# Kernel optimization log

Hardware: AMD Instinct MI355X
Metric: run time of the kernel (lower is better)

The kernel has to match this reference:

```python
import jax, jax.numpy as jnp
import numpy as np

NUM_GRAPHS = 512   # number of graphs in the batch
MAX_NODES = 192    # static pad bound (actual sizes are in [96,160])
TOTAL = 65536      # total atoms across all graphs
D = 256            # model dim (from MultiheadAttention(256, 4))
H = 4              # heads
DH = D // H        # head dim = 64


def setup_inputs() -> dict:
    # Ragged graph sizes that sum exactly to TOTAL (pairs 128+p / 128-p).
    rng = np.random.default_rng(0)
    p = rng.integers(0, 33, size=NUM_GRAPHS // 2)
    sizes = np.concatenate([128 + p, 128 - p])
    rng.shuffle(sizes)
    batch = np.repeat(np.arange(NUM_GRAPHS, dtype=np.int32), sizes)

    key = jax.random.key(0)
    ks = jax.random.split(key, 12)
    s = 0.02
    return {
        "x": jax.random.normal(ks[0], (TOTAL, D), jnp.float32),
        "batch": jnp.asarray(batch),
        # attn1 (torch MultiheadAttention packed in_proj + out_proj)
        "in_w1": jax.random.normal(ks[1], (3 * D, D), jnp.float32) * s,
        "in_b1": jnp.zeros((3 * D,), jnp.float32),
        "out_w1": jax.random.normal(ks[2], (D, D), jnp.float32) * s,
        "out_b1": jnp.zeros((D,), jnp.float32),
        # attn2
        "in_w2": jax.random.normal(ks[3], (3 * D, D), jnp.float32) * s,
        "in_b2": jnp.zeros((3 * D,), jnp.float32),
        "out_w2": jax.random.normal(ks[4], (D, D), jnp.float32) * s,
        "out_b2": jnp.zeros((D,), jnp.float32),
        # readout MLP: 256 -> 256 -> 128 -> 1 (dropout is identity in eval)
        "r_w1": jax.random.normal(ks[5], (256, 256), jnp.float32) * s,
        "r_b1": jnp.zeros((256,), jnp.float32),
        "r_w2": jax.random.normal(ks[6], (128, 256), jnp.float32) * s,
        "r_b2": jnp.zeros((128,), jnp.float32),
        "r_w3": jax.random.normal(ks[7], (1, 128), jnp.float32) * s,
        "r_b3": jnp.zeros((1,), jnp.float32),
    }


def _mha(xd, mask, in_w, in_b, out_w, out_b):
    # xd: [B, L, D], mask: [B, L] (True = valid key). torch MHA semantics.
    B, L, _ = xd.shape
    qkv = xd @ in_w.T + in_b                                  # [B, L, 3D]
    q, k, v = jnp.split(qkv, 3, axis=-1)
    split = lambda t: t.reshape(B, L, H, DH).transpose(0, 2, 1, 3)  # [B,H,L,DH]
    q, k, v = split(q), split(k), split(v)
    scores = jnp.einsum("bhqd,bhkd->bhqk", q, k) / jnp.sqrt(jnp.float32(DH))
    scores = jnp.where(mask[:, None, None, :], scores, -jnp.inf)
    attn = jax.nn.softmax(scores, axis=-1)                    # each graph has >=1 node
    o = jnp.einsum("bhqk,bhkd->bhqd", attn, v)                # [B,H,L,DH]
    o = o.transpose(0, 2, 1, 3).reshape(B, L, D)
    return o @ out_w.T + out_b


def reference(x, batch, in_w1, in_b1, out_w1, out_b1,
              in_w2, in_b2, out_w2, out_b2,
              r_w1, r_b1, r_w2, r_b2, r_w3, r_b3):
    # Scatter ragged atoms into a padded dense [B, MAX_NODES, D] block
    # (equivalent to the per-graph Python loop, but one fused pass).
    idx = jnp.arange(TOTAL)
    pos = idx - jnp.searchsorted(batch, batch, side="left")   # position within graph
    dense = jnp.zeros((NUM_GRAPHS, MAX_NODES, D), x.dtype).at[batch, pos].set(x)
    mask = jnp.zeros((NUM_GRAPHS, MAX_NODES), bool).at[batch, pos].set(True)

    h = _mha(dense, mask, in_w1, in_b1, out_w1, out_b1)
    h = _mha(h, mask, in_w2, in_b2, out_w2, out_b2)

    # masked mean-pool over valid nodes of each graph
    m = mask[..., None].astype(h.dtype)
    pooled = (h * m).sum(axis=1) / m.sum(axis=1)              # [B, D]

    h1 = jax.nn.relu(pooled @ r_w1.T + r_b1)                  # dropout = identity (eval)
    h2 = jax.nn.relu(h1 @ r_w2.T + r_b2)
    energy = h2 @ r_w3.T + r_b3                               # [B, 1]
    return energy[:, 0]                                       # (batch_size,)
```

## Files before the change

kernel.cpp:

```cpp
#include <hip/hip_runtime.h>
#include <math.h>

#define TOTAL 65536
#define NG 512
#define DMODEL 256
#define QKVLD 768

typedef __attribute__((ext_vector_type(8))) short bf16x8;
typedef __attribute__((ext_vector_type(4))) float f32x4;

__device__ inline ushort f2bf(float f) {
    unsigned int u = __float_as_uint(f);
    unsigned int r = (u + 0x7FFFu + ((u >> 16) & 1u)) >> 16;
    return (ushort)r;
}
__device__ inline float bf2f(ushort h) { return __uint_as_float(((unsigned int)h) << 16); }

__device__ __forceinline__ void llds16(const void* gptr, void* lptr) {
    __builtin_amdgcn_global_load_lds(
        (const __attribute__((address_space(1))) unsigned int*)gptr,
        (__attribute__((address_space(3))) unsigned int*)lptr, 16, 0, 0);
}

__global__ __launch_bounds__(256) void prep_kernel(
    const float* __restrict__ x, const float* __restrict__ in_w1,
    const float* __restrict__ in_w2, const float* __restrict__ out_w1,
    const float* __restrict__ out_b1, const float* __restrict__ in_b2,
    const int* __restrict__ batch,
    ushort* __restrict__ xb, ushort* __restrict__ Wb1,
    ushort* __restrict__ Wc2b, float* __restrict__ bc2, int* __restrict__ starts)
{
    const int b = blockIdx.x, t = threadIdx.x;
    if (b < 16384) {
        int i = b * 256 + t;
        float4 v = ((const float4*)x)[i];
        ushort4 u;
        u.x = f2bf(v.x); u.y = f2bf(v.y); u.z = f2bf(v.z); u.w = f2bf(v.w);
        ((ushort4*)xb)[i] = u;
    } else if (b < 16576) {
        int i = (b - 16384) * 256 + t;
        float4 v = ((const float4*)in_w1)[i];
        ushort4 u;
        u.x = f2bf(v.x); u.y = f2bf(v.y); u.z = f2bf(v.z); u.w = f2bf(v.w);
        ((ushort4*)Wb1)[i] = u;
    } else if (b < 17344) {
        const int n = b - 16576;
        __shared__ float wrow[256];
        wrow[t] = in_w2[n * 256 + t];
        __syncthreads();
        float s = 0.f;
#pragma unroll 8
        for (int j = 0; j < 256; ++j) s += wrow[j] * out_w1[j * 256 + t];
        Wc2b[n * 256 + t] = f2bf(s);
    } else if (b < 17347) {
        int n = (b - 17344) * 256 + t;
        if (n < 768) {
            float s = 0.f;
            for (int j = 0; j < 256; ++j) s += in_w2[n * 256 + j] * out_b1[j];
            bc2[n] = s + in_b2[n];
        }
    } else {
        int g = (b - 17347) * 256 + t;
        if (g < NG) {
            int lo = 0, hi = TOTAL;
            while (lo < hi) {
                int mid = (lo + hi) >> 1;
                if (batch[mid] < g) lo = mid + 1; else hi = mid;
            }
            starts[g] = lo;
            if (g == 0) starts[NG] = TOTAL;
        }
    }
}

__global__ __launch_bounds__(256) void gemm_mfma(
    const ushort* __restrict__ A,
    const ushort* __restrict__ W,
    const float* __restrict__ bias,
    ushort* __restrict__ C, int ldc)
{
    __shared__ ushort As[128 * 64];
    __shared__ ushort Bs[128 * 64];
    const int tid = threadIdx.x;
    const int lane = tid & 63, wid = tid >> 6;
    const int grp = lane >> 4, ln16 = lane & 15;
    const int wm = wid & 1, wn = wid >> 1;
    const int n0 = blockIdx.x * 128, m0 = blockIdx.y * 128;

    const int lrow = lane >> 3;
    const int lchunk = (lane & 7) ^ lrow;

    f32x4 acc[4][4];
#pragma unroll
    for (int i = 0; i < 4; ++i)
#pragma unroll
        for (int j = 0; j < 4; ++j) acc[i][j] = (f32x4){0.f, 0.f, 0.f, 0.f};

    for (int k0 = 0; k0 < 256; k0 += 64) {
#pragma unroll
        for (int j = 0; j < 4; ++j) {
            int band = wid * 32 + j * 8;
            int row = band + lrow;
            llds16(A + (size_t)(m0 + row) * 256 + k0 + lchunk * 8, &As[band * 64]);
            llds16(W + (size_t)(n0 + row) * 256 + k0 + lchunk * 8, &Bs[band * 64]);
        }
        __syncthreads();
#pragma unroll
        for (int kc = 0; kc < 2; ++kc) {
            bf16x8 a[4], b[4];
#pragma unroll
            for (int i = 0; i < 4; ++i) {
                int r = wm * 64 + i * 16 + ln16;
                int p = (kc * 4 + grp) ^ (r & 7);
                a[i] = *(const bf16x8*)&As[r * 64 + p * 8];
            }
#pragma unroll
            for (int j = 0; j < 4; ++j) {
                int r = wn * 64 + j * 16 + ln16;
                int p = (kc * 4 + grp) ^ (r & 7);
                b[j] = *(const bf16x8*)&Bs[r * 64 + p * 8];
            }
#pragma unroll
            for (int i = 0; i < 4; ++i)
#pragma unroll
                for (int j = 0; j < 4; ++j)
                    acc[i][j] = __builtin_amdgcn_mfma_f32_16x16x32_bf16(a[i], b[j], acc[i][j], 0, 0, 0);
        }
        __syncthreads();
    }

#pragma unroll
    for (int j = 0; j < 4; ++j) {
        int col = n0 + wn * 64 + j * 16 + ln16;
        float bv = bias[col];
#pragma unroll
        for (int i = 0; i < 4; ++i) {
            int r0 = m0 + wm * 64 + i * 16 + grp * 4;
#pragma unroll
            for (int reg = 0; reg < 4; ++reg)
                C[(size_t)(r0 + reg) * ldc + col] = f2bf(acc[i][j][reg] + bv);
        }
    }
}

#define VLD 168
#define PLD 72

__global__ __launch_bounds__(256) void attn_mfma(const ushort* __restrict__ qkv,
                                                 ushort* __restrict__ obuf,
                                                 float* __restrict__ psumOut,
                                                 const int* __restrict__ starts) {
    __shared__ ushort Ks[160 * 64];
    __shared__ ushort Vt[64 * VLD];
    __shared__ ushort Ps[4 * 16 * PLD];
    __shared__ float  red[4][64];
    const int g = blockIdx.x;
    const int h = blockIdx.y;
    int s = starts[g];
    int e = starts[g + 1];
    s = (s < 0) ? 0 : ((s > TOTAL) ? TOTAL : s);
    e = (e < s) ? s : ((e > TOTAL) ? TOTAL : e);
    int L = e - s;
    if (L > 160) L = 160;
    if (L < 1) L = 1;
    const int tid = threadIdx.x;
    const int lane = tid & 63, wid = tid >> 6;
    const int grp = lane >> 4, ln16 = lane & 15;
    const int lrow = lane >> 3;
    const int lchunk = (lane & 7) ^ lrow;

#pragma unroll
    for (int r = 0; r < 5; ++r) {
        int band = (r * 4 + wid) * 8;
        int row = band + lrow;
        int crow = (row < L) ? row : (L - 1);
        llds16(qkv + (size_t)(s + crow) * QKVLD + 256 + h * 64 + lchunk * 8, &Ks[band * 64]);
    }
#pragma unroll
    for (int r = 0; r < 5; ++r) {
        int idx = r * 256 + tid;
        int kc = idx >> 6;
        int d = idx & 63;
        ushort tmp[8];
#pragma unroll
        for (int j = 0; j < 8; ++j) {
            int key = kc * 8 + j;
            int ckey = (key < L) ? key : (L - 1);
            tmp[j] = qkv[(size_t)(s + ckey) * QKVLD + 512 + h * 64 + d];
        }
        *(uint4*)&Vt[d * VLD + kc * 8] = *(const uint4*)tmp;
    }
    __syncthreads();

    ushort* myP = &Ps[wid * 16 * PLD];
    float psum[4] = {0.f, 0.f, 0.f, 0.f};
    const bool pooled = (psumOut != nullptr);

    for (int q0 = wid * 16; q0 < L; q0 += 64) {
        bf16x8 qa[2];
        {
            int qi = q0 + ln16;
            int grow = (qi < L) ? (s + qi) : s;
            const ushort* qbase = qkv + (size_t)grow * QKVLD + h * 64;
            qa[0] = *(const bf16x8*)(qbase + grp * 8);
            qa[1] = *(const bf16x8*)(qbase + 32 + grp * 8);
        }
        f32x4 sc[10];
#pragma unroll
        for (int kt = 0; kt < 10; ++kt) {
            int row = kt * 16 + ln16;
            int p0 = grp ^ (row & 7);
            int p1 = (4 + grp) ^ (row & 7);
            bf16x8 b0 = *(const bf16x8*)&Ks[row * 64 + p0 * 8];
            bf16x8 b1 = *(const bf16x8*)&Ks[row * 64 + p1 * 8];
            f32x4 z = (f32x4){0.f, 0.f, 0.f, 0.f};
            z = __builtin_amdgcn_mfma_f32_16x16x32_bf16(qa[0], b0, z, 0, 0, 0);
            z = __builtin_amdgcn_mfma_f32_16x16x32_bf16(qa[1], b1, z, 0, 0, 0);
            sc[kt] = z;
        }
        float sm[4] = {0.f, 0.f, 0.f, 0.f};
#pragma unroll
        for (int kt = 0; kt < 10; ++kt) {
            bool dead = (kt * 16 + ln16) >= L;
#pragma unroll
            for (int r = 0; r < 4; ++r) {
                float p = __expf(dead ? -INFINITY : sc[kt][r] * 0.125f);
                sc[kt][r] = p;
                sm[r] += p;
            }
        }
#pragma unroll
        for (int m = 1; m <= 8; m <<= 1)
#pragma unroll
            for (int r = 0; r < 4; ++r) sm[r] += __shfl_xor(sm[r], m, 64);
        float inv[4];
#pragma unroll
        for (int r = 0; r < 4; ++r) inv[r] = 1.f / sm[r];

        f32x4 o[4];
#pragma unroll
        for (int dt = 0; dt < 4; ++dt) o[dt] = (f32x4){0.f, 0.f, 0.f, 0.f};
#pragma unroll
        for (int st = 0; st < 3; ++st) {
            const int nkt = (st == 2) ? 2 : 4;
            const int nkc = (st == 2) ? 1 : 2;
#pragma unroll
            for (int kti = 0; kti < 4; ++kti) {
                if (kti < nkt) {
                    int kt = st * 4 + kti;
#pragma unroll
                    for (int r = 0; r < 4; ++r)
                        myP[(grp * 4 + r) * PLD + kti * 16 + ln16] = f2bf(sc[kt][r]);
                }
            }
#pragma unroll
            for (int kc2 = 0; kc2 < 2; ++kc2) {
                if (kc2 < nkc) {
                    bf16x8 pa = *(const bf16x8*)&myP[ln16 * PLD + kc2 * 32 + grp * 8];
                    int kcg = st * 2 + kc2;
#pragma unroll
                    for (int dt = 0; dt < 4; ++dt) {
                        bf16x8 vb = *(const bf16x8*)&Vt[(dt * 16 + ln16) * VLD + kcg * 32 + grp * 8];
                        o[dt] = __builtin_amdgcn_mfma_f32_16x16x32_bf16(pa, vb, o[dt], 0, 0, 0);
                    }
                }
            }
        }
        if (pooled) {
#pragma unroll
            for (int dt = 0; dt < 4; ++dt)
#pragma unroll
                for (int reg = 0; reg < 4; ++reg) {
                    int q = q0 + grp * 4 + reg;
                    if (q < L) psum[dt] += o[dt][reg] * inv[reg];
                }
        } else {
#pragma unroll
            for (int dt = 0; dt < 4; ++dt)
#pragma unroll
                for (int reg = 0; reg < 4; ++reg) {
                    int q = q0 + grp * 4 + reg;
                    if (q < L)
                        obuf[(size_t)(s + q) * DMODEL + h * 64 + dt * 16 + ln16] =
                            f2bf(o[dt][reg] * inv[reg]);
                }
        }
    }

    if (pooled) {
#pragma unroll
        for (int dt = 0; dt < 4; ++dt) {
            psum[dt] += __shfl_xor(psum[dt], 16, 64);
            psum[dt] += __shfl_xor(psum[dt], 32, 64);
        }
        if (grp == 0) {
#pragma unroll
            for (int dt = 0; dt < 4; ++dt) red[wid][dt * 16 + ln16] = psum[dt];
        }
        __syncthreads();
        if (tid < 64) {
            float v = red[0][tid] + red[1][tid] + red[2][tid] + red[3][tid];
            psumOut[g * DMODEL + h * 64 + tid] = v;
        }
    }
}

__global__ __launch_bounds__(256) void readout_kernel(
    const float* __restrict__ psum, const int* __restrict__ starts,
    const float* __restrict__ ow2, const float* __restrict__ ob2,
    const float* __restrict__ w1, const float* __restrict__ b1,
    const float* __restrict__ w2, const float* __restrict__ b2,
    const float* __restrict__ w3, const float* __restrict__ b3,
    float* __restrict__ out)
{
    __shared__ float xs[256], ps[256], h1s[256], h2s[128];
    const int g = blockIdx.x, t = threadIdx.x;
    int s = starts[g], e = starts[g + 1];
    s = (s < 0) ? 0 : ((s > TOTAL) ? TOTAL : s);
    e = (e < s) ? s : ((e > TOTAL) ? TOTAL : e);
    int L = e - s;
    if (L < 1) L = 1;
    xs[t] = psum[g * 256 + t] / (float)L;
    __syncthreads();
    {
        const float* wr = ow2 + t * 256;
        float s0 = 0.f;
#pragma unroll 8
        for (int i = 0; i < 256; ++i) s0 += xs[i] * wr[i];
        ps[t] = s0 + ob2[t];
    }
    __syncthreads();
    {
        const float* wr = w1 + t * 256;
        float s0 = 0.f;
#pragma unroll 8
        for (int i = 0; i < 256; ++i) s0 += ps[i] * wr[i];
        float v = s0 + b1[t];
        h1s[t] = v > 0.f ? v : 0.f;
    }
    __syncthreads();
    if (t < 128) {
        const float* wr = w2 + t * 256;
        float s0 = 0.f;
#pragma unroll 8
        for (int i = 0; i < 256; ++i) s0 += h1s[i] * wr[i];
        float v = s0 + b2[t];
        h2s[t] = v > 0.f ? v : 0.f;
    }
    __syncthreads();
    if (t < 64) {
        float v = h2s[t] * w3[t] + h2s[t + 64] * w3[t + 64];
#pragma unroll
        for (int off = 32; off > 0; off >>= 1) v += __shfl_down(v, off, 64);
        if (t == 0) out[g] = v + b3[0];
    }
}

__global__ __launch_bounds__(256) void zero_out_kernel(float* __restrict__ out, int n) {
    int i = blockIdx.x * 256 + threadIdx.x;
    if (i < n) out[i] = 0.f;
}

extern "C" void kernel_launch(void* const* d_in, const int* in_sizes, int n_in,
                              void* d_out, int out_size, void* d_ws, size_t ws_size,
                              hipStream_t stream) {
    float* out = (float*)d_out;

    const int expect[16] = {
        TOTAL * DMODEL, TOTAL,
        3 * DMODEL * DMODEL, 3 * DMODEL,
        DMODEL * DMODEL, DMODEL,
        3 * DMODEL * DMODEL, 3 * DMODEL,
        DMODEL * DMODEL, DMODEL,
        256 * 256, 256,
        128 * 256, 128,
        128, 1
    };
    const size_t NEEDED = 135536640ull;
    bool ok = (n_in == 16) && (out_size == NG) && (d_ws != nullptr) && (ws_size >= NEEDED);
    if (ok) {
        for (int i = 0; i < 16; ++i)
            if (in_sizes[i] != expect[i]) { ok = false; break; }
    }
    if (!ok) {
        zero_out_kernel<<<(out_size + 255) / 256, 256, 0, stream>>>(out, out_size);
        return;
    }

    const float* x      = (const float*)d_in[0];
    const int*   batch  = (const int*)d_in[1];
    const float* in_w1  = (const float*)d_in[2];
    const float* in_b1  = (const float*)d_in[3];
    const float* out_w1 = (const float*)d_in[4];
    const float* out_b1 = (const float*)d_in[5];
    const float* in_w2  = (const float*)d_in[6];
    const float* in_b2  = (const float*)d_in[7];
    const float* out_w2 = (const float*)d_in[8];
    const float* out_b2 = (const float*)d_in[9];
    const float* r_w1   = (const float*)d_in[10];
    const float* r_b1   = (const float*)d_in[11];
    const float* r_w2   = (const float*)d_in[12];
    const float* r_b2   = (const float*)d_in[13];
    const float* r_w3   = (const float*)d_in[14];
    const float* r_b3   = (const float*)d_in[15];

    char* ws = (char*)d_ws;
    int*    starts = (int*)(ws + 0);
    float*  bc2    = (float*)(ws + 4096);
    float*  psum   = (float*)(ws + 8192);
    ushort* Wc2b   = (ushort*)(ws + 532480);
    ushort* Wb1    = (ushort*)(ws + 925696);
    ushort* bufO   = (ushort*)(ws + 1318912);
    ushort* bufQKV = (ushort*)(ws + 34873344ull);

    prep_kernel<<<17349, 256, 0, stream>>>(x, in_w1, in_w2, out_w1, out_b1, in_b2,
                                           batch, bufO, Wb1, Wc2b, bc2, starts);

    gemm_mfma<<<dim3(6, 512), 256, 0, stream>>>(bufO, Wb1, in_b1, bufQKV, QKVLD);
    attn_mfma<<<dim3(NG, 4), 256, 0, stream>>>(bufQKV, bufO, nullptr, starts);

    gemm_mfma<<<dim3(6, 512), 256, 0, stream>>>(bufO, Wc2b, bc2, bufQKV, QKVLD);
    attn_mfma<<<dim3(NG, 4), 256, 0, stream>>>(bufQKV, bufO, psum, starts);

    readout_kernel<<<NG, 256, 0, stream>>>(psum, starts, out_w2, out_b2,
                                           r_w1, r_b1, r_w2, r_b2, r_w3, r_b3, out);
}
```

Baseline: 377.0 us.

## Keep full A row-tile resident in LDS and loop over all N tiles per block

The QKV GEMM now loads each block's entire 128x256 A tile into LDS once and iterates over all six 128-column output tiles inside the block. Weight fragments are read straight from global memory into registers instead of being staged through LDS. This removes the sixfold re-reading of A across a 6x512 grid and the per-k-step barriers. In exchange the grid shrinks to 512 blocks, LDS use grows to 64KB per block (lowering occupancy), and B loads become uncached, latency-exposed global reads inside the MFMA loop.

```diff
diff --git a/kernel.cpp b/kernel.cpp
--- a/kernel.cpp
+++ b/kernel.cpp
@@ -79,66 +79,66 @@
     const float* __restrict__ bias,
     ushort* __restrict__ C, int ldc)
 {
-    __shared__ ushort As[128 * 64];
-    __shared__ ushort Bs[128 * 64];
+    __shared__ ushort As[128 * 256];
     const int tid = threadIdx.x;
     const int lane = tid & 63, wid = tid >> 6;
     const int grp = lane >> 4, ln16 = lane & 15;
     const int wm = wid & 1, wn = wid >> 1;
-    const int n0 = blockIdx.x * 128, m0 = blockIdx.y * 128;
-
-    const int lrow = lane >> 3;
-    const int lchunk = (lane & 7) ^ lrow;
-
-    f32x4 acc[4][4];
-#pragma unroll
-    for (int i = 0; i < 4; ++i)
-#pragma unroll
-        for (int j = 0; j < 4; ++j) acc[i][j] = (f32x4){0.f, 0.f, 0.f, 0.f};
-
-    for (int k0 = 0; k0 < 256; k0 += 64) {
+    const int m0 = blockIdx.x * 128;
+
+#pragma unroll
+    for (int rr = 0; rr < 16; ++rr) {
+        int blk = wid * 16 + rr;
+        int row = blk * 2 + (lane >> 5);
+        int csrc = (lane & 31) ^ (row & 7);
+        llds16(A + (size_t)(m0 + row) * 256 + csrc * 8, &As[blk * 512]);
+    }
+    __syncthreads();
+
+    for (int nt = 0; nt < 6; ++nt) {
+        const int n0 = nt * 128;
+        f32x4 acc[4][4];
+#pragma unroll
+        for (int i = 0; i < 4; ++i)
+#pragma unroll
+            for (int j = 0; j < 4; ++j) acc[i][j] = (f32x4){0.f, 0.f, 0.f, 0.f};
+
+        for (int k0 = 0; k0 < 256; k0 += 64) {
+#pragma unroll
+            for (int kc = 0; kc < 2; ++kc) {
+                bf16x8 a[4], b[4];
+#pragma unroll
+                for (int i = 0; i < 4; ++i) {
+                    int r = wm * 64 + i * 16 + ln16;
+                    int c = (k0 >> 3) + kc * 4 + grp;
+                    int p = c ^ (r & 7);
+                    a[i] = *(const bf16x8*)&As[r * 256 + p * 8];
+                }
+#pragma unroll
+                for (int j = 0; j < 4; ++j) {
+                    const ushort* wp = W + (size_t)(n0 + wn * 64 + j * 16 + ln16) * 256
+                                         + k0 + kc * 32 + grp * 8;
+                    b[j] = *(const bf16x8*)wp;
+                }
+#pragma unroll
+                for (int i = 0; i < 4; ++i)
+#pragma unroll
+                    for (int j = 0; j < 4; ++j)
+                        acc[i][j] = __builtin_amdgcn_mfma_f32_16x16x32_bf16(a[i], b[j], acc[i][j], 0, 0, 0);
+            }
+        }
+
 #pragma unroll
         for (int j = 0; j < 4; ++j) {
-            int band = wid * 32 + j * 8;
-            int row = band + lrow;
-            llds16(A + (size_t)(m0 + row) * 256 + k0 + lchunk * 8, &As[band * 64]);
-            llds16(W + (size_t)(n0 + row) * 256 + k0 + lchunk * 8, &Bs[band * 64]);
-        }
-        __syncthreads();
-#pragma unroll
-        for (int kc = 0; kc < 2; ++kc) {
-            bf16x8 a[4], b[4];
+            int col = n0 + wn * 64 + j * 16 + ln16;
+            float bv = bias[col];
 #pragma unroll
             for (int i = 0; i < 4; ++i) {
-                int r = wm * 64 + i * 16 + ln16;
-                int p = (kc * 4 + grp) ^ (r & 7);
-                a[i] = *(const bf16x8*)&As[r * 64 + p * 8];
-            }
-#pragma unroll
-            for (int j = 0; j < 4; ++j) {
-                int r = wn * 64 + j * 16 + ln16;
-                int p = (kc * 4 + grp) ^ (r & 7);
-                b[j] = *(const bf16x8*)&Bs[r * 64 + p * 8];
-            }
-#pragma unroll
-            for (int i = 0; i < 4; ++i)
-#pragma unroll
-                for (int j = 0; j < 4; ++j)
-                    acc[i][j] = __builtin_amdgcn_mfma_f32_16x16x32_bf16(a[i], b[j], acc[i][j], 0, 0, 0);
-        }
-        __syncthreads();
-    }
-
-#pragma unroll
-    for (int j = 0; j < 4; ++j) {
-        int col = n0 + wn * 64 + j * 16 + ln16;
-        float bv = bias[col];
-#pragma unroll
-        for (int i = 0; i < 4; ++i) {
-            int r0 = m0 + wm * 64 + i * 16 + grp * 4;
-#pragma unroll
-            for (int reg = 0; reg < 4; ++reg)
-                C[(size_t)(r0 + reg) * ldc + col] = f2bf(acc[i][j][reg] + bv);
+                int r0 = m0 + wm * 64 + i * 16 + grp * 4;
+#pragma unroll
+                for (int reg = 0; reg < 4; ++reg)
+                    C[(size_t)(r0 + reg) * ldc + col] = f2bf(acc[i][j][reg] + bv);
+            }
         }
     }
 }
@@ -416,10 +416,10 @@
     prep_kernel<<<17349, 256, 0, stream>>>(x, in_w1, in_w2, out_w1, out_b1, in_b2,
                                            batch, bufO, Wb1, Wc2b, bc2, starts);
 
-    gemm_mfma<<<dim3(6, 512), 256, 0, stream>>>(bufO, Wb1, in_b1, bufQKV, QKVLD);
+    gemm_mfma<<<dim3(512), 256, 0, stream>>>(bufO, Wb1, in_b1, bufQKV, QKVLD);
     attn_mfma<<<dim3(NG, 4), 256, 0, stream>>>(bufQKV, bufO, nullptr, starts);
 
-    gemm_mfma<<<dim3(6, 512), 256, 0, stream>>>(bufO, Wc2b, bc2, bufQKV, QKVLD);
+    gemm_mfma<<<dim3(512), 256, 0, stream>>>(bufO, Wc2b, bc2, bufQKV, QKVLD);
     attn_mfma<<<dim3(NG, 4), 256, 0, stream>>>(bufQKV, bufO, psum, starts);
 
     readout_kernel<<<NG, 256, 0, stream>>>(psum, starts, out_w2, out_b2,
```

After: 402.8 us. 6.8% more time.
